# Kernel tuning notes

Measured on AMD Instinct MI355X. Metric: run time of the kernel, lower is better.

The kernel has to match this reference:

```python
import jax, jax.numpy as jnp
import numpy as np

DIM = 512
HEADS = 8
DIM_HEAD = 32
INNER = HEADS * DIM_HEAD  # 256
B, N = 2, 2048
EPS = 1e-5


def setup_inputs() -> dict:
    key = jax.random.key(0)
    ks = jax.random.split(key, 6)
    x = jax.random.normal(ks[0], (B, N, DIM), dtype=jnp.float32)
    rel_pos_bias = jax.random.normal(ks[1], (HEADS, N, N), dtype=jnp.float32)
    ln_scale = jnp.ones((DIM,), dtype=jnp.float32)
    w_qkv = jax.random.normal(ks[2], (DIM, INNER * 3), dtype=jnp.float32) / np.sqrt(DIM)
    w_out = jax.random.normal(ks[3], (INNER, DIM), dtype=jnp.float32) / np.sqrt(INNER)
    b_out = jnp.zeros((DIM,), dtype=jnp.float32)
    return {"x": x, "rel_pos_bias": rel_pos_bias, "ln_scale": ln_scale,
            "w_qkv": w_qkv, "w_out": w_out, "b_out": b_out}


def reference(x, rel_pos_bias, ln_scale, w_qkv, w_out, b_out):
    scale = DIM_HEAD ** -0.5
    # LayerNorm (no bias), eps=1e-5
    mu = jnp.mean(x, axis=-1, keepdims=True)
    var = jnp.mean(jnp.square(x - mu), axis=-1, keepdims=True)
    xn = (x - mu) * jax.lax.rsqrt(var + EPS) * ln_scale
    # fused QKV projection, no bias
    qkv = xn @ w_qkv  # [b, n, 3*inner]
    q, k, v = jnp.split(qkv, 3, axis=-1)
    def to_heads(t):
        b, n, _ = t.shape
        return t.reshape(b, n, HEADS, DIM_HEAD).transpose(0, 2, 1, 3)  # b h n d
    q, k, v = map(to_heads, (q, k, v))
    q = q * scale
    sim = jnp.einsum('bhid,bhjd->bhij', q, k)
    sim = sim + rel_pos_bias  # (h,n,n) broadcasts over batch
    attn = jax.nn.softmax(sim, axis=-1)
    o = jnp.einsum('bhij,bhjd->bhid', attn, v)
    o = o.transpose(0, 2, 1, 3).reshape(x.shape[0], x.shape[1], INNER)  # b n (h d)
    return o @ w_out + b_out
```

## Files before the change

kernel.cpp:

```cpp
#include <hip/hip_runtime.h>
#include <hip/hip_bf16.h>
#include <cstdint>

#define NB 2
#define NSEQ 2048
#define NDIM 512
#define NHEAD 8
#define DHEAD 32
#define NINNER 256
#define NQKV 768
#define LNEPS 1e-5f
#define QSCALE 0.17677669529663687f

typedef short short8 __attribute__((ext_vector_type(8)));
typedef float f32x4 __attribute__((ext_vector_type(4)));
typedef unsigned int u32x4 __attribute__((ext_vector_type(4)));
typedef unsigned int u32x2 __attribute__((ext_vector_type(2)));
typedef unsigned short u16;
typedef unsigned int u32;

__device__ __forceinline__ f32x4 mfma16(short8 a, short8 b, f32x4 c) {
    return __builtin_amdgcn_mfma_f32_16x16x32_bf16(a, b, c, 0, 0, 0);
}

__device__ __forceinline__ u16 f2bf(float a) {
    union { float f; u32 u; } x; x.f = a;
    u32 r = x.u + 0x7fffu + ((x.u >> 16) & 1u);
    return (u16)(r >> 16);
}
__device__ __forceinline__ float bf2f(u16 h) {
    union { float f; u32 u; } x; x.u = ((u32)h) << 16; return x.f;
}
__device__ __forceinline__ void split2(float a, u16& hi, u16& lo) {
    hi = f2bf(a);
    lo = f2bf(a - bf2f(hi));
}
__device__ __forceinline__ u32 pk2(float a, float b) {
    return (u32)f2bf(a) | ((u32)f2bf(b) << 16);
}

__global__ __launch_bounds__(256) void ln_kernel(
    const float* __restrict__ x, const float* __restrict__ gamma,
    u32* __restrict__ xn_hi, u32* __restrict__ xn_lo)
{
    const int row = blockIdx.x;
    const int t = threadIdx.x;
    const float2 v = ((const float2*)(x + (size_t)row * NDIM))[t];
    float s1 = v.x + v.y;
    float s2 = v.x * v.x + v.y * v.y;
    #pragma unroll
    for (int off = 32; off >= 1; off >>= 1) {
        s1 += __shfl_down(s1, off);
        s2 += __shfl_down(s2, off);
    }
    __shared__ float a1[4], a2[4];
    if ((t & 63) == 0) { a1[t >> 6] = s1; a2[t >> 6] = s2; }
    __syncthreads();
    const float ts1 = a1[0] + a1[1] + a1[2] + a1[3];
    const float ts2 = a2[0] + a2[1] + a2[2] + a2[3];
    const float mu = ts1 * (1.0f / NDIM);
    const float var = ts2 * (1.0f / NDIM) - mu * mu;
    const float rs = rsqrtf(var + LNEPS);
    const float2 g = ((const float2*)gamma)[t];
    u16 h0, l0, h1, l1;
    split2((v.x - mu) * rs * g.x, h0, l0);
    split2((v.y - mu) * rs * g.y, h1, l1);
    xn_hi[(size_t)row * (NDIM / 2) + t] = (u32)h0 | ((u32)h1 << 16);
    xn_lo[(size_t)row * (NDIM / 2) + t] = (u32)l0 | ((u32)l1 << 16);
}

__global__ __launch_bounds__(256) void wtrans_kernel(
    const float* __restrict__ wq, u16* __restrict__ wqT_hi, u16* __restrict__ wqT_lo,
    const float* __restrict__ wo, u16* __restrict__ woT_hi, u16* __restrict__ woT_lo)
{
    __shared__ __align__(16) u16 th[64][72], tl[64][72];
    const int t = threadIdx.x;
    const float* w; u16 *wT_hi, *wT_lo; int K, N, k0, n0;
    if (blockIdx.x < 96) {
        w = wq; wT_hi = wqT_hi; wT_lo = wqT_lo; K = NDIM; N = NQKV;
        k0 = (blockIdx.x & 7) * 64; n0 = (blockIdx.x >> 3) * 64;
    } else {
        const int b = blockIdx.x - 96;
        w = wo; wT_hi = woT_hi; wT_lo = woT_lo; K = NINNER; N = NDIM;
        k0 = (b & 3) * 64; n0 = (b >> 2) * 64;
    }
    {
        const int k = t >> 2, c = (t & 3) * 16;
        const float* src = w + (size_t)(k0 + k) * N + n0 + c;
        #pragma unroll
        for (int jj = 0; jj < 4; jj++) {
            const f32x4 w4 = *(const f32x4*)(src + jj * 4);
            #pragma unroll
            for (int e = 0; e < 4; e++) {
                u16 hh, ll;
                split2(w4[e], hh, ll);
                th[k][c + jj * 4 + e] = hh;
                tl[k][c + jj * 4 + e] = ll;
            }
        }
    }
    __syncthreads();
    {
        const int n = t >> 2, kc = (t & 3) * 16;
        u16 hb[16], lb[16];
        #pragma unroll
        for (int j = 0; j < 16; j++) { hb[j] = th[kc + j][n]; lb[j] = tl[kc + j][n]; }
        u16* dh = wT_hi + (size_t)(n0 + n) * K + k0 + kc;
        u16* dl = wT_lo + (size_t)(n0 + n) * K + k0 + kc;
        *(short8*)dh = *(short8*)hb;
        *(short8*)(dh + 8) = *(short8*)(hb + 8);
        *(short8*)dl = *(short8*)lb;
        *(short8*)(dl + 8) = *(short8*)(lb + 8);
    }
}

__global__ __launch_bounds__(256) void vtrans_kernel(
    const u16* __restrict__ v, u16* __restrict__ vt)
{
    __shared__ __align__(16) u16 sh[64][40];
    const int t = threadIdx.x;
    const int n0 = blockIdx.x * 64;
    const int bh = blockIdx.y;
    {
        const int n = t >> 2, c = (t & 3) * 8;
        *(short8*)&sh[n][c] = *(const short8*)(v + ((size_t)bh * NSEQ + n0 + n) * DHEAD + c);
    }
    __syncthreads();
    {
        const int d = t >> 3, nc = (t & 7) * 8;
        u16 buf[8];
        #pragma unroll
        for (int j = 0; j < 8; j++) buf[j] = sh[nc + j][d];
        *(short8*)(vt + ((size_t)bh * DHEAD + d) * NSEQ + n0 + nc) = *(short8*)buf;
    }
}

__global__ __launch_bounds__(256, 4) void qkv_kernel(
    const u16* __restrict__ xn_hi, const u16* __restrict__ xn_lo,
    const u16* __restrict__ wT_hi, const u16* __restrict__ wT_lo,
    u16* __restrict__ q_hi, u16* __restrict__ q_lo,
    u16* __restrict__ k_hi, u16* __restrict__ k_lo,
    u16* __restrict__ v)
{
    __shared__ __align__(16) u16 Ah[64][40], Al[64][40], Bh[64][40], Bl[64][40];
    const int t = threadIdx.x;
    const int wave = t >> 6, lane = t & 63;
    const int lrow = lane & 15, lquad = lane >> 4;
    const int rowBase = blockIdx.x * 64;
    const int colBase = blockIdx.y * 64;
    const int wm = (wave & 1) * 32;
    const int wn = (wave >> 1) * 32;
    const int kf = lquad * 8;
    const f32x4 zero = {0.f, 0.f, 0.f, 0.f};
    f32x4 acc[2][2];
    acc[0][0] = zero; acc[0][1] = zero; acc[1][0] = zero; acc[1][1] = zero;

    const int sr = t >> 2, sc = (t & 3) * 8;

    for (int k0 = 0; k0 < NDIM; k0 += 32) {
        __syncthreads();
        *(short8*)&Ah[sr][sc] = *(const short8*)(xn_hi + (size_t)(rowBase + sr) * NDIM + k0 + sc);
        *(short8*)&Al[sr][sc] = *(const short8*)(xn_lo + (size_t)(rowBase + sr) * NDIM + k0 + sc);
        *(short8*)&Bh[sr][sc] = *(const short8*)(wT_hi + (size_t)(colBase + sr) * NDIM + k0 + sc);
        *(short8*)&Bl[sr][sc] = *(const short8*)(wT_lo + (size_t)(colBase + sr) * NDIM + k0 + sc);
        __syncthreads();
        const short8 a0h = *(const short8*)&Ah[wm + lrow][kf];
        const short8 a0l = *(const short8*)&Al[wm + lrow][kf];
        const short8 a1h = *(const short8*)&Ah[wm + 16 + lrow][kf];
        const short8 a1l = *(const short8*)&Al[wm + 16 + lrow][kf];
        const short8 b0h = *(const short8*)&Bh[wn + lrow][kf];
        const short8 b0l = *(const short8*)&Bl[wn + lrow][kf];
        const short8 b1h = *(const short8*)&Bh[wn + 16 + lrow][kf];
        const short8 b1l = *(const short8*)&Bl[wn + 16 + lrow][kf];
        acc[0][0] = mfma16(a0h, b0h, acc[0][0]); acc[0][0] = mfma16(a0h, b0l, acc[0][0]); acc[0][0] = mfma16(a0l, b0h, acc[0][0]);
        acc[0][1] = mfma16(a0h, b1h, acc[0][1]); acc[0][1] = mfma16(a0h, b1l, acc[0][1]); acc[0][1] = mfma16(a0l, b1h, acc[0][1]);
        acc[1][0] = mfma16(a1h, b0h, acc[1][0]); acc[1][0] = mfma16(a1h, b0l, acc[1][0]); acc[1][0] = mfma16(a1l, b0h, acc[1][0]);
        acc[1][1] = mfma16(a1h, b1h, acc[1][1]); acc[1][1] = mfma16(a1h, b1l, acc[1][1]); acc[1][1] = mfma16(a1l, b1h, acc[1][1]);
    }

    #pragma unroll
    for (int mi = 0; mi < 2; mi++) {
        #pragma unroll
        for (int ni = 0; ni < 2; ni++) {
            #pragma unroll
            for (int r = 0; r < 4; r++) {
                const int grow = rowBase + wm + mi * 16 + lquad * 4 + r;
                const int gcol = colBase + wn + ni * 16 + lrow;
                const float val = acc[mi][ni][r];
                const int bidx = grow >> 11;
                const int n = grow & (NSEQ - 1);
                const int sec = gcol >> 8;
                const int idx = gcol & 255;
                const int head = idx >> 5, d = idx & 31;
                const int bh = bidx * NHEAD + head;
                if (sec == 0) {
                    u16 hh, ll;
                    split2(val * QSCALE, hh, ll);
                    const size_t a = ((size_t)bh * NSEQ + n) * DHEAD + d;
                    q_hi[a] = hh; q_lo[a] = ll;
                } else if (sec == 1) {
                    u16 hh, ll;
                    split2(val, hh, ll);
                    const size_t a = ((size_t)bh * NSEQ + n) * DHEAD + d;
                    k_hi[a] = hh; k_lo[a] = ll;
                } else {
                    v[((size_t)bh * NSEQ + n) * DHEAD + d] = f2bf(val);
                }
            }
        }
    }
}

__global__ __launch_bounds__(512, 4) void attn_kernel(
    const u16* __restrict__ q_hi, const u16* __restrict__ q_lo,
    const u16* __restrict__ k_hi, const u16* __restrict__ k_lo,
    const u16* __restrict__ vt,
    const float* __restrict__ bias,
    u16* __restrict__ o_hi, u16* __restrict__ o_lo)
{
    __shared__ __align__(16) float cA[2][2][4][64][4];
    __shared__ __align__(16) float cB[2][2][4][64][4];
    __shared__ float cl[2][2][4][16];
    const int t = threadIdx.x;
    const int wave = t >> 6, lane = t & 63;
    const int lrow = lane & 15, lquad = lane >> 4;
    const int qpair = wave & 1, kslice = wave >> 1;
    const int bh = blockIdx.y;
    const int batch = bh >> 3, head = bh & 7;
    const int qb = blockIdx.x * 64 + qpair * 32;
    const size_t qkb = (size_t)bh * NSEQ * DHEAD;
    const size_t qoff0 = (size_t)(qb + lrow) * DHEAD + lquad * 8;
    const size_t qoff1 = (size_t)(qb + 16 + lrow) * DHEAD + lquad * 8;
    const short8 qh0 = *(const short8*)(q_hi + qkb + qoff0);
    const short8 ql0 = *(const short8*)(q_lo + qkb + qoff0);
    const short8 qh1 = *(const short8*)(q_hi + qkb + qoff1);
    const short8 ql1 = *(const short8*)(q_lo + qkb + qoff1);
    const f32x4 zero = {0.f, 0.f, 0.f, 0.f};
    f32x4 accA0 = zero, accB0 = zero, accA1 = zero, accB1 = zero;
    float lp0 = 0.f, lp1 = 0.f;
    const int kperm = ((lrow >> 2) << 3) | (lrow & 3);
    const float* bptr0 = bias + (size_t)head * NSEQ * NSEQ + (size_t)(qb + lrow) * NSEQ;
    const float* bptr1 = bptr0 + 16 * NSEQ;
    const int kt0 = kslice * 512;

    f32x4 b00 = *(const f32x4*)(bptr0 + kt0 + lquad * 8);
    f32x4 b01 = *(const f32x4*)(bptr0 + kt0 + lquad * 8 + 4);
    f32x4 b10 = *(const f32x4*)(bptr1 + kt0 + lquad * 8);
    f32x4 b11 = *(const f32x4*)(bptr1 + kt0 + lquad * 8 + 4);

    for (int i = 0; i < 16; i++) {
        const int kt = kt0 + i * 32;
        const size_t kof = (size_t)(kt + kperm) * DHEAD + lquad * 8;
        const short8 k0h = *(const short8*)(k_hi + qkb + kof);
        const short8 k0l = *(const short8*)(k_lo + qkb + kof);
        const short8 k1h = *(const short8*)(k_hi + qkb + kof + 4 * DHEAD);
        const short8 k1l = *(const short8*)(k_lo + qkb + kof + 4 * DHEAD);
        const short8 va0 = *(const short8*)(vt + qkb + (size_t)lrow * NSEQ + kt + lquad * 8);
        const short8 va1 = *(const short8*)(vt + qkb + (size_t)(16 + lrow) * NSEQ + kt + lquad * 8);
        const int ktn = kt0 + ((i + 1) & 15) * 32;
        const f32x4 nb00 = *(const f32x4*)(bptr0 + ktn + lquad * 8);
        const f32x4 nb01 = *(const f32x4*)(bptr0 + ktn + lquad * 8 + 4);
        const f32x4 nb10 = *(const f32x4*)(bptr1 + ktn + lquad * 8);
        const f32x4 nb11 = *(const f32x4*)(bptr1 + ktn + lquad * 8 + 4);

        {
            f32x4 c0 = zero, c1 = zero;
            c0 = mfma16(k0h, qh0, c0); c0 = mfma16(k0h, ql0, c0); c0 = mfma16(k0l, qh0, c0);
            c1 = mfma16(k1h, qh0, c1); c1 = mfma16(k1h, ql0, c1); c1 = mfma16(k1l, qh0, c1);
            f32x4 p0, p1;
            #pragma unroll
            for (int r = 0; r < 4; r++) {
                p0[r] = __expf(c0[r] + b00[r]);
                p1[r] = __expf(c1[r] + b01[r]);
            }
            lp0 += (p0[0] + p0[1]) + (p0[2] + p0[3]) + (p1[0] + p1[1]) + (p1[2] + p1[3]);
            union { u32x4 u; short8 s; } cv;
            cv.u[0] = pk2(p0[0], p0[1]);
            cv.u[1] = pk2(p0[2], p0[3]);
            cv.u[2] = pk2(p1[0], p1[1]);
            cv.u[3] = pk2(p1[2], p1[3]);
            accA0 = mfma16(va0, cv.s, accA0);
            accB0 = mfma16(va1, cv.s, accB0);
        }
        {
            f32x4 c0 = zero, c1 = zero;
            c0 = mfma16(k0h, qh1, c0); c0 = mfma16(k0h, ql1, c0); c0 = mfma16(k0l, qh1, c0);
            c1 = mfma16(k1h, qh1, c1); c1 = mfma16(k1h, ql1, c1); c1 = mfma16(k1l, qh1, c1);
            f32x4 p0, p1;
            #pragma unroll
            for (int r = 0; r < 4; r++) {
                p0[r] = __expf(c0[r] + b10[r]);
                p1[r] = __expf(c1[r] + b11[r]);
            }
            lp1 += (p0[0] + p0[1]) + (p0[2] + p0[3]) + (p1[0] + p1[1]) + (p1[2] + p1[3]);
            union { u32x4 u; short8 s; } cv;
            cv.u[0] = pk2(p0[0], p0[1]);
            cv.u[1] = pk2(p0[2], p0[3]);
            cv.u[2] = pk2(p1[0], p1[1]);
            cv.u[3] = pk2(p1[2], p1[3]);
            accA1 = mfma16(va0, cv.s, accA1);
            accB1 = mfma16(va1, cv.s, accB1);
        }
        b00 = nb00; b01 = nb01; b10 = nb10; b11 = nb11;
    }

    lp0 += __shfl_xor(lp0, 16); lp0 += __shfl_xor(lp0, 32);
    lp1 += __shfl_xor(lp1, 16); lp1 += __shfl_xor(lp1, 32);

    *(f32x4*)&cA[qpair][0][kslice][lane][0] = accA0;
    *(f32x4*)&cB[qpair][0][kslice][lane][0] = accB0;
    *(f32x4*)&cA[qpair][1][kslice][lane][0] = accA1;
    *(f32x4*)&cB[qpair][1][kslice][lane][0] = accB1;
    if (lquad == 0) {
        cl[qpair][0][kslice][lrow] = lp0;
        cl[qpair][1][kslice][lrow] = lp1;
    }
    __syncthreads();
    if (wave < 4) {
        const int qp = wave >> 1, s = wave & 1;
        f32x4 sA = *(const f32x4*)&cA[qp][s][0][lane][0];
        f32x4 sB = *(const f32x4*)&cB[qp][s][0][lane][0];
        #pragma unroll
        for (int w = 1; w < 4; w++) {
            sA += *(const f32x4*)&cA[qp][s][w][lane][0];
            sB += *(const f32x4*)&cB[qp][s][w][lane][0];
        }
        const float lt = cl[qp][s][0][lrow] + cl[qp][s][1][lrow]
                       + cl[qp][s][2][lrow] + cl[qp][s][3][lrow];
        const float inv = 1.0f / lt;
        const int q = blockIdx.x * 64 + qp * 32 + s * 16 + lrow;
        const size_t base = ((size_t)batch * NSEQ + q) * NINNER + head * DHEAD + lquad * 4;
        u16 h[8], l[8];
        #pragma unroll
        for (int r = 0; r < 4; r++) {
            split2(sA[r] * inv, h[r], l[r]);
            split2(sB[r] * inv, h[4 + r], l[4 + r]);
        }
        *(u32x2*)&o_hi[base] = *(u32x2*)&h[0];
        *(u32x2*)&o_hi[base + 16] = *(u32x2*)&h[4];
        *(u32x2*)&o_lo[base] = *(u32x2*)&l[0];
        *(u32x2*)&o_lo[base + 16] = *(u32x2*)&l[4];
    }
}

__global__ __launch_bounds__(256, 4) void out_kernel(
    const u16* __restrict__ o_hi, const u16* __restrict__ o_lo,
    const u16* __restrict__ wT_hi, const u16* __restrict__ wT_lo,
    const float* __restrict__ b_out,
    float* __restrict__ out)
{
    __shared__ __align__(16) u16 Ah[64][40], Al[64][40], Bh[64][40], Bl[64][40];
    const int t = threadIdx.x;
    const int wave = t >> 6, lane = t & 63;
    const int lrow = lane & 15, lquad = lane >> 4;
    const int rowBase = blockIdx.x * 64;
    const int colBase = blockIdx.y * 64;
    const int wm = (wave & 1) * 32;
    const int wn = (wave >> 1) * 32;
    const int kf = lquad * 8;
    const f32x4 zero = {0.f, 0.f, 0.f, 0.f};
    f32x4 acc[2][2];
    acc[0][0] = zero; acc[0][1] = zero; acc[1][0] = zero; acc[1][1] = zero;

    const int sr = t >> 2, sc = (t & 3) * 8;

    for (int k0 = 0; k0 < NINNER; k0 += 32) {
        __syncthreads();
        *(short8*)&Ah[sr][sc] = *(const short8*)(o_hi + (size_t)(rowBase + sr) * NINNER + k0 + sc);
        *(short8*)&Al[sr][sc] = *(const short8*)(o_lo + (size_t)(rowBase + sr) * NINNER + k0 + sc);
        *(short8*)&Bh[sr][sc] = *(const short8*)(wT_hi + (size_t)(colBase + sr) * NINNER + k0 + sc);
        *(short8*)&Bl[sr][sc] = *(const short8*)(wT_lo + (size_t)(colBase + sr) * NINNER + k0 + sc);
        __syncthreads();
        const short8 a0h = *(const short8*)&Ah[wm + lrow][kf];
        const short8 a0l = *(const short8*)&Al[wm + lrow][kf];
        const short8 a1h = *(const short8*)&Ah[wm + 16 + lrow][kf];
        const short8 a1l = *(const short8*)&Al[wm + 16 + lrow][kf];
        const short8 b0h = *(const short8*)&Bh[wn + lrow][kf];
        const short8 b0l = *(const short8*)&Bl[wn + lrow][kf];
        const short8 b1h = *(const short8*)&Bh[wn + 16 + lrow][kf];
        const short8 b1l = *(const short8*)&Bl[wn + 16 + lrow][kf];
        acc[0][0] = mfma16(a0h, b0h, acc[0][0]); acc[0][0] = mfma16(a0h, b0l, acc[0][0]); acc[0][0] = mfma16(a0l, b0h, acc[0][0]);
        acc[0][1] = mfma16(a0h, b1h, acc[0][1]); acc[0][1] = mfma16(a0h, b1l, acc[0][1]); acc[0][1] = mfma16(a0l, b1h, acc[0][1]);
        acc[1][0] = mfma16(a1h, b0h, acc[1][0]); acc[1][0] = mfma16(a1h, b0l, acc[1][0]); acc[1][0] = mfma16(a1l, b0h, acc[1][0]);
        acc[1][1] = mfma16(a1h, b1h, acc[1][1]); acc[1][1] = mfma16(a1h, b1l, acc[1][1]); acc[1][1] = mfma16(a1l, b1h, acc[1][1]);
    }

    #pragma unroll
    for (int mi = 0; mi < 2; mi++) {
        #pragma unroll
        for (int ni = 0; ni < 2; ni++) {
            #pragma unroll
            for (int r = 0; r < 4; r++) {
                const int grow = rowBase + wm + mi * 16 + lquad * 4 + r;
                const int gcol = colBase + wn + ni * 16 + lrow;
                out[(size_t)grow * NDIM + gcol] = acc[mi][ni][r] + b_out[gcol];
            }
        }
    }
}

extern "C" void kernel_launch(void* const* d_in, const int* in_sizes, int n_in,
                              void* d_out, int out_size, void* d_ws, size_t ws_size,
                              hipStream_t stream)
{
    (void)in_sizes; (void)n_in; (void)out_size; (void)ws_size;
    const float* x     = (const float*)d_in[0];
    const float* bias  = (const float*)d_in[1];
    const float* gamma = (const float*)d_in[2];
    const float* wqkv  = (const float*)d_in[3];
    const float* wout  = (const float*)d_in[4];
    const float* bout  = (const float*)d_in[5];
    float* out = (float*)d_out;

    char* ws = (char*)d_ws;
    size_t off = 0;
    auto carve = [&](size_t bytes) -> void* {
        void* p = (void*)(ws + off);
        off += (bytes + 255) & ~(size_t)255;
        return p;
    };
    const size_t rows = (size_t)NB * NSEQ;
    const size_t hn = (size_t)NB * NHEAD * NSEQ * DHEAD;
    u16* xn_hi = (u16*)carve(rows * NDIM * 2);
    u16* xn_lo = (u16*)carve(rows * NDIM * 2);
    u16* wqT_hi = (u16*)carve((size_t)NQKV * NDIM * 2);
    u16* wqT_lo = (u16*)carve((size_t)NQKV * NDIM * 2);
    u16* woT_hi = (u16*)carve((size_t)NDIM * NINNER * 2);
    u16* woT_lo = (u16*)carve((size_t)NDIM * NINNER * 2);
    u16* q_hi  = (u16*)carve(hn * 2);
    u16* q_lo  = (u16*)carve(hn * 2);
    u16* k_hi  = (u16*)carve(hn * 2);
    u16* k_lo  = (u16*)carve(hn * 2);
    u16* vbuf  = (u16*)carve(hn * 2);
    u16* vt    = (u16*)carve(hn * 2);
    u16* o_hi  = (u16*)carve(rows * NINNER * 2);
    u16* o_lo  = (u16*)carve(rows * NINNER * 2);

    ln_kernel<<<dim3((unsigned)rows), 256, 0, stream>>>(x, gamma, (u32*)xn_hi, (u32*)xn_lo);
    wtrans_kernel<<<dim3(128), 256, 0, stream>>>(wqkv, wqT_hi, wqT_lo, wout, woT_hi, woT_lo);
    qkv_kernel<<<dim3(64, 12), 256, 0, stream>>>(xn_hi, xn_lo, wqT_hi, wqT_lo,
                                                 q_hi, q_lo, k_hi, k_lo, vbuf);
    vtrans_kernel<<<dim3(NSEQ / 64, NB * NHEAD), 256, 0, stream>>>(vbuf, vt);
    attn_kernel<<<dim3(32, 16), 512, 0, stream>>>(q_hi, q_lo, k_hi, k_lo,
                                                  vt, bias, o_hi, o_lo);
    out_kernel<<<dim3(64, 8), 256, 0, stream>>>(o_hi, o_lo, woT_hi, woT_lo, bout, out);
}
```

Baseline: 276.5 us.

## Split attention block over eight key slices with 32 queries per block

Each attention block now covers 32 queries instead of 64, and its eight waves each handle a 256-key slice rather than a 2x4 query-pair/key-slice arrangement. The grid doubles to 64x16 blocks, which is meant to improve occupancy and load balance across the GPU's compute units. The final reduction sums eight partial accumulators, and four waves each write half of a 16-row output. The cost is more cross-wave reduction traffic through shared memory and shorter per-wave loops, so the bias prefetch pipeline covers fewer iterations.

```diff
diff --git a/kernel.cpp b/kernel.cpp
--- a/kernel.cpp
+++ b/kernel.cpp
@@ -218,16 +218,16 @@
     const float* __restrict__ bias,
     u16* __restrict__ o_hi, u16* __restrict__ o_lo)
 {
-    __shared__ __align__(16) float cA[2][2][4][64][4];
-    __shared__ __align__(16) float cB[2][2][4][64][4];
-    __shared__ float cl[2][2][4][16];
+    __shared__ __align__(16) float cA[2][8][64][4];
+    __shared__ __align__(16) float cB[2][8][64][4];
+    __shared__ float cl[2][8][16];
     const int t = threadIdx.x;
     const int wave = t >> 6, lane = t & 63;
     const int lrow = lane & 15, lquad = lane >> 4;
-    const int qpair = wave & 1, kslice = wave >> 1;
+    const int kslice = wave;
     const int bh = blockIdx.y;
     const int batch = bh >> 3, head = bh & 7;
-    const int qb = blockIdx.x * 64 + qpair * 32;
+    const int qb = blockIdx.x * 32;
     const size_t qkb = (size_t)bh * NSEQ * DHEAD;
     const size_t qoff0 = (size_t)(qb + lrow) * DHEAD + lquad * 8;
     const size_t qoff1 = (size_t)(qb + 16 + lrow) * DHEAD + lquad * 8;
@@ -241,14 +241,14 @@
     const int kperm = ((lrow >> 2) << 3) | (lrow & 3);
     const float* bptr0 = bias + (size_t)head * NSEQ * NSEQ + (size_t)(qb + lrow) * NSEQ;
     const float* bptr1 = bptr0 + 16 * NSEQ;
-    const int kt0 = kslice * 512;
+    const int kt0 = kslice * 256;
 
     f32x4 b00 = *(const f32x4*)(bptr0 + kt0 + lquad * 8);
     f32x4 b01 = *(const f32x4*)(bptr0 + kt0 + lquad * 8 + 4);
     f32x4 b10 = *(const f32x4*)(bptr1 + kt0 + lquad * 8);
     f32x4 b11 = *(const f32x4*)(bptr1 + kt0 + lquad * 8 + 4);
 
-    for (int i = 0; i < 16; i++) {
+    for (int i = 0; i < 8; i++) {
         const int kt = kt0 + i * 32;
         const size_t kof = (size_t)(kt + kperm) * DHEAD + lquad * 8;
         const short8 k0h = *(const short8*)(k_hi + qkb + kof);
@@ -257,7 +257,7 @@
         const short8 k1l = *(const short8*)(k_lo + qkb + kof + 4 * DHEAD);
         const short8 va0 = *(const short8*)(vt + qkb + (size_t)lrow * NSEQ + kt + lquad * 8);
         const short8 va1 = *(const short8*)(vt + qkb + (size_t)(16 + lrow) * NSEQ + kt + lquad * 8);
-        const int ktn = kt0 + ((i + 1) & 15) * 32;
+        const int ktn = kt0 + ((i + 1) & 7) * 32;
         const f32x4 nb00 = *(const f32x4*)(bptr0 + ktn + lquad * 8);
         const f32x4 nb01 = *(const f32x4*)(bptr0 + ktn + lquad * 8 + 4);
         const f32x4 nb10 = *(const f32x4*)(bptr1 + ktn + lquad * 8);
@@ -307,39 +307,37 @@
     lp0 += __shfl_xor(lp0, 16); lp0 += __shfl_xor(lp0, 32);
     lp1 += __shfl_xor(lp1, 16); lp1 += __shfl_xor(lp1, 32);
 
-    *(f32x4*)&cA[qpair][0][kslice][lane][0] = accA0;
-    *(f32x4*)&cB[qpair][0][kslice][lane][0] = accB0;
-    *(f32x4*)&cA[qpair][1][kslice][lane][0] = accA1;
-    *(f32x4*)&cB[qpair][1][kslice][lane][0] = accB1;
+    *(f32x4*)&cA[0][kslice][lane][0] = accA0;
+    *(f32x4*)&cB[0][kslice][lane][0] = accB0;
+    *(f32x4*)&cA[1][kslice][lane][0] = accA1;
+    *(f32x4*)&cB[1][kslice][lane][0] = accB1;
     if (lquad == 0) {
-        cl[qpair][0][kslice][lrow] = lp0;
-        cl[qpair][1][kslice][lrow] = lp1;
+        cl[0][kslice][lrow] = lp0;
+        cl[1][kslice][lrow] = lp1;
     }
     __syncthreads();
     if (wave < 4) {
-        const int qp = wave >> 1, s = wave & 1;
-        f32x4 sA = *(const f32x4*)&cA[qp][s][0][lane][0];
-        f32x4 sB = *(const f32x4*)&cB[qp][s][0][lane][0];
-        #pragma unroll
-        for (int w = 1; w < 4; w++) {
-            sA += *(const f32x4*)&cA[qp][s][w][lane][0];
-            sB += *(const f32x4*)&cB[qp][s][w][lane][0];
-        }
-        const float lt = cl[qp][s][0][lrow] + cl[qp][s][1][lrow]
-                       + cl[qp][s][2][lrow] + cl[qp][s][3][lrow];
+        const int s = wave >> 1, part = wave & 1;
+        const float (*src)[64][4] = part ? (const float (*)[64][4])cB[s]
+                                         : (const float (*)[64][4])cA[s];
+        f32x4 sv = *(const f32x4*)&src[0][lane][0];
+        #pragma unroll
+        for (int w = 1; w < 8; w++) {
+            sv += *(const f32x4*)&src[w][lane][0];
+        }
+        float lt = 0.f;
+        #pragma unroll
+        for (int w = 0; w < 8; w++) lt += cl[s][w][lrow];
         const float inv = 1.0f / lt;
-        const int q = blockIdx.x * 64 + qp * 32 + s * 16 + lrow;
-        const size_t base = ((size_t)batch * NSEQ + q) * NINNER + head * DHEAD + lquad * 4;
-        u16 h[8], l[8];
+        const int q = qb + s * 16 + lrow;
+        const size_t base = ((size_t)batch * NSEQ + q) * NINNER + head * DHEAD + part * 16 + lquad * 4;
+        u16 h[4], l[4];
         #pragma unroll
         for (int r = 0; r < 4; r++) {
-            split2(sA[r] * inv, h[r], l[r]);
-            split2(sB[r] * inv, h[4 + r], l[4 + r]);
+            split2(sv[r] * inv, h[r], l[r]);
         }
         *(u32x2*)&o_hi[base] = *(u32x2*)&h[0];
-        *(u32x2*)&o_hi[base + 16] = *(u32x2*)&h[4];
         *(u32x2*)&o_lo[base] = *(u32x2*)&l[0];
-        *(u32x2*)&o_lo[base + 16] = *(u32x2*)&l[4];
     }
 }
 
@@ -441,7 +439,7 @@
     qkv_kernel<<<dim3(64, 12), 256, 0, stream>>>(xn_hi, xn_lo, wqT_hi, wqT_lo,
                                                  q_hi, q_lo, k_hi, k_lo, vbuf);
     vtrans_kernel<<<dim3(NSEQ / 64, NB * NHEAD), 256, 0, stream>>>(vbuf, vt);
-    attn_kernel<<<dim3(32, 16), 512, 0, stream>>>(q_hi, q_lo, k_hi, k_lo,
-                                                  vt, bias, o_hi, o_lo);
+    attn_kernel<<<dim3(NSEQ / 32, NB * NHEAD), 512, 0, stream>>>(q_hi, q_lo, k_hi, k_lo,
+                                                                 vt, bias, o_hi, o_lo);
     out_kernel<<<dim3(64, 8), 256, 0, stream>>>(o_hi, o_lo, woT_hi, woT_lo, bout, out);
 }
```

New measurement: 280.3 us. No clear change (+1.4%).
